# Kernel optimization log

Hardware: AMD Instinct MI355X
Metric: run time of the kernel (lower is better)

Reference implementation:

```python
import jax, jax.numpy as jnp
import numpy as np

WINDOW_SIZE = 11
SIGMA = 1.5
C1 = 0.01 ** 2
C2 = 0.03 ** 2


def _gaussian_window(channels):
    coords = jnp.arange(WINDOW_SIZE, dtype=jnp.float32) - WINDOW_SIZE // 2
    g = jnp.exp(-coords ** 2 / (2.0 * SIGMA ** 2))
    g = g / g.sum()
    w2d = g[:, None] * g[None, :]                      # [K, K]
    # depthwise kernel: [out_ch=C, in_ch/groups=1, K, K]
    return jnp.broadcast_to(w2d[None, None], (channels, 1, WINDOW_SIZE, WINDOW_SIZE))


def _depthwise_conv(x, window):
    # x: [B, C, H, W]; grouped conv with feature_group_count = C, SAME padding
    C = x.shape[1]
    pad = WINDOW_SIZE // 2
    return jax.lax.conv_general_dilated(
        x, window,
        window_strides=(1, 1),
        padding=((pad, pad), (pad, pad)),
        dimension_numbers=("NCHW", "OIHW", "NCHW"),
        feature_group_count=C,
    )


def setup_inputs() -> dict:
    key = jax.random.key(0)
    k1, k2 = jax.random.split(key)
    shape = (16, 3, 512, 512)
    pred = jax.random.uniform(k1, shape, dtype=jnp.float32)
    target = jax.random.uniform(k2, shape, dtype=jnp.float32)
    return {"pred": pred, "target": target}


def reference(pred, target):
    C = pred.shape[1]
    window = _gaussian_window(C)
    mu_p = _depthwise_conv(pred, window)
    mu_t = _depthwise_conv(target, window)
    mu_p_sq = mu_p ** 2
    mu_t_sq = mu_t ** 2
    mu_cross = mu_p * mu_t
    sigma_p_sq = _depthwise_conv(pred ** 2, window) - mu_p_sq
    sigma_t_sq = _depthwise_conv(target ** 2, window) - mu_t_sq
    sigma_cross = _depthwise_conv(pred * target, window) - mu_cross
    ssim_map = ((2.0 * mu_cross + C1) * (2.0 * sigma_cross + C2)) / (
        (mu_p_sq + mu_t_sq + C1) * (sigma_p_sq + sigma_t_sq + C2)
    )
    return 1.0 - ssim_map.mean()
```

## Files before the change

### kernel.cpp

```cpp
#include <hip/hip_runtime.h>

#define HH 512
#define WW 512
#define NPLANE 48
#define BY 128
#define CHK 16
#define NCH (BY / CHK)
#define SLOTS 40
#define ALLOC 42
#define KS 11

typedef __attribute__((ext_vector_type(8))) short short8;
typedef __attribute__((ext_vector_type(4))) float floatx4;

__device__ inline unsigned pk2bf_rne(float a, float b) {
    union { float f; unsigned u; } ua, ub;
    ua.f = a; ub.f = b;
    unsigned lo = (ua.u + 0x7FFFu + ((ua.u >> 16) & 1u)) >> 16;
    unsigned hi = (ub.u + 0x7FFFu + ((ub.u >> 16) & 1u)) >> 16;
    return lo | (hi << 16);
}

__device__ inline unsigned pkhu(float a, float b) {
    union { float f; unsigned u; } ua, ub;
    ua.f = a; ub.f = b;
    return __builtin_amdgcn_perm(ub.u + 0x8000u, ua.u + 0x8000u, 0x07060302u);
}

__global__ __launch_bounds__(256, 4) void ssim_kernel(
    const float* __restrict__ pred, const float* __restrict__ target,
    float* __restrict__ ws_sum)
{
    __shared__ __align__(16) short ring[4][5][16][ALLOC];
    __shared__ float red[4];

    const int tid = threadIdx.x;
    const int wv = tid >> 6;
    const int lane = tid & 63;
    const int m = lane & 15;
    const int quad = lane >> 4;

    float wsum = 0.f;
#pragma unroll
    for (int k = 0; k < KS; ++k) {
        float d = (float)(k - 5);
        wsum += __expf(-d * d * (1.0f / 4.5f));
    }
    const float invs = 1.0f / wsum;

    short8 Wf;
    {
        union { short8 v; unsigned u[4]; } W;
#pragma unroll
        for (int jj = 0; jj < 4; ++jj) {
            float v0, v1;
            {
                int idx = quad * 8 + 2 * jj - m - 3;
                float d = (float)(idx - 5);
                v0 = (idx >= 0 && idx < KS) ? __expf(-d * d * (1.0f / 4.5f)) * invs : 0.f;
            }
            {
                int idx = quad * 8 + 2 * jj + 1 - m - 3;
                float d = (float)(idx - 5);
                v1 = (idx >= 0 && idx < KS) ? __expf(-d * d * (1.0f / 4.5f)) * invs : 0.f;
            }
            W.u[jj] = pk2bf_rne(v0, v1);
        }
        Wf = W.v;
    }

    const size_t poff = (size_t)blockIdx.z * HH * WW;
    const float* __restrict__ pp = pred + poff;
    const float* __restrict__ tp = target + poff;
    const int X0 = blockIdx.x * 64 + wv * 16;
    const int rawX = X0 - 8;
    const int Y0 = blockIdx.y * BY;

    const float C1 = 1.0e-4f;
    const float C2 = 9.0e-4f;
    float lsum = 0.f;
    const floatx4 z = {0.f, 0.f, 0.f, 0.f};

    auto h_step = [&](int k, int sb) {
        const int row = Y0 + CHK * k - 8 + m;
        const bool rowok = ((unsigned)row < (unsigned)HH);
        const int c0 = rawX + quad * 8;
        float4 p0 = {0, 0, 0, 0}, p1 = {0, 0, 0, 0};
        float4 t0 = {0, 0, 0, 0}, t1 = {0, 0, 0, 0};
        if (rowok) {
            const float* pr = pp + (size_t)row * WW;
            const float* tr = tp + (size_t)row * WW;
            if ((unsigned)c0 < (unsigned)WW) {
                p0 = *(const float4*)(pr + c0);
                t0 = *(const float4*)(tr + c0);
            }
            if ((unsigned)(c0 + 4) < (unsigned)WW) {
                p1 = *(const float4*)(pr + c0 + 4);
                t1 = *(const float4*)(tr + c0 + 4);
            }
        }
        const float p[8] = {p0.x, p0.y, p0.z, p0.w, p1.x, p1.y, p1.z, p1.w};
        const float t[8] = {t0.x, t0.y, t0.z, t0.w, t1.x, t1.y, t1.z, t1.w};
        union { short8 v; unsigned u[4]; } Fp, Ft, Fpp, Ftt, Fpt;
#pragma unroll
        for (int jj = 0; jj < 4; ++jj) {
            const float a0 = p[2 * jj], a1 = p[2 * jj + 1];
            const float b0 = t[2 * jj], b1 = t[2 * jj + 1];
            Fp.u[jj]  = pkhu(a0, a1);
            Ft.u[jj]  = pkhu(b0, b1);
            Fpp.u[jj] = pkhu(a0 * a0, a1 * a1);
            Ftt.u[jj] = pkhu(b0 * b0, b1 * b1);
            Fpt.u[jj] = pkhu(a0 * b0, a1 * b1);
        }
        floatx4 Dp  = __builtin_amdgcn_mfma_f32_16x16x32_bf16(Fp.v,  Wf, z, 0, 0, 0);
        floatx4 Dt  = __builtin_amdgcn_mfma_f32_16x16x32_bf16(Ft.v,  Wf, z, 0, 0, 0);
        floatx4 Dpp = __builtin_amdgcn_mfma_f32_16x16x32_bf16(Fpp.v, Wf, z, 0, 0, 0);
        floatx4 Dtt = __builtin_amdgcn_mfma_f32_16x16x32_bf16(Ftt.v, Wf, z, 0, 0, 0);
        floatx4 Dpt = __builtin_amdgcn_mfma_f32_16x16x32_bf16(Fpt.v, Wf, z, 0, 0, 0);
        int slot = sb + quad * 4;
        if (slot >= SLOTS) slot -= SLOTS;
        {
            uint2 v;
            v.x = pkhu(Dp[0], Dp[1]);   v.y = pkhu(Dp[2], Dp[3]);
            *(uint2*)&ring[wv][0][m][slot] = v;
            v.x = pkhu(Dt[0], Dt[1]);   v.y = pkhu(Dt[2], Dt[3]);
            *(uint2*)&ring[wv][1][m][slot] = v;
            v.x = pkhu(Dpp[0], Dpp[1]); v.y = pkhu(Dpp[2], Dpp[3]);
            *(uint2*)&ring[wv][2][m][slot] = v;
            v.x = pkhu(Dtt[0], Dtt[1]); v.y = pkhu(Dtt[2], Dtt[3]);
            *(uint2*)&ring[wv][3][m][slot] = v;
            v.x = pkhu(Dpt[0], Dpt[1]); v.y = pkhu(Dpt[2], Dpt[3]);
            *(uint2*)&ring[wv][4][m][slot] = v;
        }
    };

    auto v_step = [&](int vb) {
        int sq = vb + quad * 8;
        if (sq >= SLOTS) sq -= SLOTS;
        const short8 Bp  = *(const short8*)&ring[wv][0][m][sq];
        const short8 Bt  = *(const short8*)&ring[wv][1][m][sq];
        const short8 Bpp = *(const short8*)&ring[wv][2][m][sq];
        const short8 Btt = *(const short8*)&ring[wv][3][m][sq];
        const short8 Bpt = *(const short8*)&ring[wv][4][m][sq];
        floatx4 Mp  = __builtin_amdgcn_mfma_f32_16x16x32_bf16(Wf, Bp,  z, 0, 0, 0);
        floatx4 Mt  = __builtin_amdgcn_mfma_f32_16x16x32_bf16(Wf, Bt,  z, 0, 0, 0);
        floatx4 Mpp = __builtin_amdgcn_mfma_f32_16x16x32_bf16(Wf, Bpp, z, 0, 0, 0);
        floatx4 Mtt = __builtin_amdgcn_mfma_f32_16x16x32_bf16(Wf, Btt, z, 0, 0, 0);
        floatx4 Mpt = __builtin_amdgcn_mfma_f32_16x16x32_bf16(Wf, Bpt, z, 0, 0, 0);
#pragma unroll
        for (int r = 0; r < 4; ++r) {
            const float mup = Mp[r], mut = Mt[r];
            const float mupsq = mup * mup, mutsq = mut * mut, mucr = mup * mut;
            const float sp2 = Mpp[r] - mupsq;
            const float st2 = Mtt[r] - mutsq;
            const float scr = Mpt[r] - mucr;
            const float n1 = 2.f * mucr + C1;
            const float n2 = 2.f * scr + C2;
            const float d1 = mupsq + mutsq + C1;
            const float d2 = sp2 + st2 + C2;
            lsum += __fdividef(n1 * n2, d1 * d2);
        }
    };

    h_step(0, (SLOTS - 8));
#pragma unroll
    for (int i = 0; i < NCH; ++i) {
        h_step(i + 1, (CHK * (i + 1) + SLOTS - 8) % SLOTS);
        v_step((CHK * i + SLOTS - 8) % SLOTS);
    }

#pragma unroll
    for (int off = 32; off > 0; off >>= 1) lsum += __shfl_down(lsum, off, 64);
    if (lane == 0) red[wv] = lsum;
    __syncthreads();
    if (tid == 0) {
        atomicAdd(ws_sum, red[0] + red[1] + red[2] + red[3]);
    }
}

__global__ void finalize_kernel(const float* __restrict__ ws_sum,
                                float* __restrict__ out) {
    out[0] = 1.0f - ws_sum[0] * (1.0f / 12582912.0f);
}

extern "C" void kernel_launch(void* const* d_in, const int* in_sizes, int n_in,
                              void* d_out, int out_size, void* d_ws, size_t ws_size,
                              hipStream_t stream) {
    const float* pred = (const float*)d_in[0];
    const float* target = (const float*)d_in[1];
    float* out = (float*)d_out;
    float* ws = (float*)d_ws;

    hipMemsetAsync(ws, 0, sizeof(float), stream);
    dim3 grid(WW / 64, HH / BY, NPLANE);
    ssim_kernel<<<grid, 256, 0, stream>>>(pred, target, ws);
    finalize_kernel<<<1, 1, 0, stream>>>(ws, out);
}
```

Measured before the change: 168.1 us.

## Software-pipeline global row loads one chunk ahead of horizontal MFMA step

```diff
diff --git a/kernel.cpp b/kernel.cpp
--- a/kernel.cpp
+++ b/kernel.cpp
@@ -7,7 +7,6 @@
 #define CHK 16
 #define NCH (BY / CHK)
 #define SLOTS 40
-#define ALLOC 42
 #define KS 11
 
 typedef __attribute__((ext_vector_type(8))) short short8;
@@ -27,11 +26,13 @@
     return __builtin_amdgcn_perm(ub.u + 0x8000u, ua.u + 0x8000u, 0x07060302u);
 }
 
+struct Raw { float4 p0, p1, t0, t1; };
+
 __global__ __launch_bounds__(256, 4) void ssim_kernel(
     const float* __restrict__ pred, const float* __restrict__ target,
     float* __restrict__ ws_sum)
 {
-    __shared__ __align__(16) short ring[4][5][16][ALLOC];
+    __shared__ __align__(16) short ring[4][5][16][SLOTS];
     __shared__ float red[4];
 
     const int tid = threadIdx.x;
@@ -81,26 +82,32 @@
     float lsum = 0.f;
     const floatx4 z = {0.f, 0.f, 0.f, 0.f};
 
-    auto h_step = [&](int k, int sb) {
+    auto load_raw = [&](int k) -> Raw {
+        Raw r;
+        r.p0 = make_float4(0, 0, 0, 0); r.p1 = make_float4(0, 0, 0, 0);
+        r.t0 = make_float4(0, 0, 0, 0); r.t1 = make_float4(0, 0, 0, 0);
         const int row = Y0 + CHK * k - 8 + m;
-        const bool rowok = ((unsigned)row < (unsigned)HH);
-        const int c0 = rawX + quad * 8;
-        float4 p0 = {0, 0, 0, 0}, p1 = {0, 0, 0, 0};
-        float4 t0 = {0, 0, 0, 0}, t1 = {0, 0, 0, 0};
-        if (rowok) {
+        if ((unsigned)row < (unsigned)HH) {
             const float* pr = pp + (size_t)row * WW;
             const float* tr = tp + (size_t)row * WW;
+            const int c0 = rawX + quad * 8;
             if ((unsigned)c0 < (unsigned)WW) {
-                p0 = *(const float4*)(pr + c0);
-                t0 = *(const float4*)(tr + c0);
+                r.p0 = *(const float4*)(pr + c0);
+                r.t0 = *(const float4*)(tr + c0);
             }
             if ((unsigned)(c0 + 4) < (unsigned)WW) {
-                p1 = *(const float4*)(pr + c0 + 4);
-                t1 = *(const float4*)(tr + c0 + 4);
-            }
-        }
-        const float p[8] = {p0.x, p0.y, p0.z, p0.w, p1.x, p1.y, p1.z, p1.w};
-        const float t[8] = {t0.x, t0.y, t0.z, t0.w, t1.x, t1.y, t1.z, t1.w};
+                r.p1 = *(const float4*)(pr + c0 + 4);
+                r.t1 = *(const float4*)(tr + c0 + 4);
+            }
+        }
+        return r;
+    };
+
+    auto h_step = [&](const Raw& r, int sb) {
+        const float p[8] = {r.p0.x, r.p0.y, r.p0.z, r.p0.w,
+                            r.p1.x, r.p1.y, r.p1.z, r.p1.w};
+        const float t[8] = {r.t0.x, r.t0.y, r.t0.z, r.t0.w,
+                            r.t1.x, r.t1.y, r.t1.z, r.t1.w};
         union { short8 v; unsigned u[4]; } Fp, Ft, Fpp, Ftt, Fpt;
 #pragma unroll
         for (int jj = 0; jj < 4; ++jj) {
@@ -119,19 +126,17 @@
         floatx4 Dpt = __builtin_amdgcn_mfma_f32_16x16x32_bf16(Fpt.v, Wf, z, 0, 0, 0);
         int slot = sb + quad * 4;
         if (slot >= SLOTS) slot -= SLOTS;
-        {
-            uint2 v;
-            v.x = pkhu(Dp[0], Dp[1]);   v.y = pkhu(Dp[2], Dp[3]);
-            *(uint2*)&ring[wv][0][m][slot] = v;
-            v.x = pkhu(Dt[0], Dt[1]);   v.y = pkhu(Dt[2], Dt[3]);
-            *(uint2*)&ring[wv][1][m][slot] = v;
-            v.x = pkhu(Dpp[0], Dpp[1]); v.y = pkhu(Dpp[2], Dpp[3]);
-            *(uint2*)&ring[wv][2][m][slot] = v;
-            v.x = pkhu(Dtt[0], Dtt[1]); v.y = pkhu(Dtt[2], Dtt[3]);
-            *(uint2*)&ring[wv][3][m][slot] = v;
-            v.x = pkhu(Dpt[0], Dpt[1]); v.y = pkhu(Dpt[2], Dpt[3]);
-            *(uint2*)&ring[wv][4][m][slot] = v;
-        }
+        uint2 v;
+        v.x = pkhu(Dp[0], Dp[1]);   v.y = pkhu(Dp[2], Dp[3]);
+        *(uint2*)&ring[wv][0][m][slot] = v;
+        v.x = pkhu(Dt[0], Dt[1]);   v.y = pkhu(Dt[2], Dt[3]);
+        *(uint2*)&ring[wv][1][m][slot] = v;
+        v.x = pkhu(Dpp[0], Dpp[1]); v.y = pkhu(Dpp[2], Dpp[3]);
+        *(uint2*)&ring[wv][2][m][slot] = v;
+        v.x = pkhu(Dtt[0], Dtt[1]); v.y = pkhu(Dtt[2], Dtt[3]);
+        *(uint2*)&ring[wv][3][m][slot] = v;
+        v.x = pkhu(Dpt[0], Dpt[1]); v.y = pkhu(Dpt[2], Dpt[3]);
+        *(uint2*)&ring[wv][4][m][slot] = v;
     };
 
     auto v_step = [&](int vb) {
@@ -162,11 +167,19 @@
         }
     };
 
-    h_step(0, (SLOTS - 8));
-#pragma unroll
+    Raw A = load_raw(0);
+    Raw B = load_raw(1);
+    int hb = SLOTS - 8;
+    int vb = SLOTS - 8;
+    h_step(A, hb);
+    hb += CHK; if (hb >= SLOTS) hb -= SLOTS;
+#pragma unroll 1
     for (int i = 0; i < NCH; ++i) {
-        h_step(i + 1, (CHK * (i + 1) + SLOTS - 8) % SLOTS);
-        v_step((CHK * i + SLOTS - 8) % SLOTS);
+        h_step(B, hb);
+        hb += CHK; if (hb >= SLOTS) hb -= SLOTS;
+        if (i + 2 <= NCH) B = load_raw(i + 2);
+        v_step(vb);
+        vb += CHK; if (vb >= SLOTS) vb -= SLOTS;
     }
 
 #pragma unroll
```

Result: faster. 142.5 us (-15.2%).
